# Kernel tuning notes

Hardware: AMD Instinct MI355X
Metric: run time of the kernel (lower is better)

Reference implementation:

```python
import jax, jax.numpy as jnp
import numpy as np

NEG_SLOPE = 0.2  # PyG GATConv leaky_relu slope
ENC_HEADS = 4


def _layernorm(x, g, b):
    mu = jnp.mean(x, axis=-1, keepdims=True)
    var = jnp.var(x, axis=-1, keepdims=True)
    return (x - mu) * jax.lax.rsqrt(var + 1e-5) * g + b


def _gat(x, src, dst, W, a_src, a_dst, bias, concat, num_nodes):
    """PyG-style GATConv: per-edge attention, scatter-softmax over dst, scatter-add."""
    heads, out = a_src.shape
    xl = (x @ W).reshape(-1, heads, out)              # (M, H, O)
    s = jnp.einsum('mho,ho->mh', xl, a_src)           # alpha_src per node
    d = jnp.einsum('mho,ho->mh', xl, a_dst)           # alpha_dst per node
    e = jax.nn.leaky_relu(s[src] + d[dst], NEG_SLOPE)  # (Etot, H)
    m = jax.lax.stop_gradient(jax.ops.segment_max(e, dst, num_segments=num_nodes))
    ee = jnp.exp(e - m[dst])
    denom = jax.ops.segment_sum(ee, dst, num_segments=num_nodes)
    alpha = ee / (denom[dst] + 1e-16)                 # scatter-softmax
    out_v = jax.ops.segment_sum(xl[src] * alpha[:, :, None], dst, num_segments=num_nodes)
    if concat:
        out_v = out_v.reshape(num_nodes, heads * out)
    else:
        out_v = out_v.mean(axis=1)
    return out_v + bias


def setup_inputs() -> dict:
    key = jax.random.key(0)
    ks = jax.random.split(key, 20)
    B, T, N, Ch, Cc = 4, 12, 10000, 8, 8
    H, GOUT, HOR, E = 128, 64, 24, 160000
    s = lambda k, shp: (jax.random.normal(k, shp, jnp.float32) * 0.05)
    return {
        'x_hist': jax.random.normal(ks[0], (B, T, N, Ch), jnp.float32),
        'x_cov': jax.random.normal(ks[1], (B, T, N, Cc), jnp.float32),
        'edge_index': jax.random.randint(ks[2], (2, E), 0, N, dtype=jnp.int32),
        'enc_in_W': s(ks[3], (Ch + Cc, H)), 'enc_in_b': jnp.zeros((H,), jnp.float32),
        'Wq': s(ks[4], (H, H)), 'Wk': s(ks[5], (H, H)), 'Wv': s(ks[6], (H, H)), 'Wo': s(ks[7], (H, H)),
        'ln1_g': jnp.ones((H,), jnp.float32), 'ln1_b': jnp.zeros((H,), jnp.float32),
        'ffn_W1': s(ks[8], (H, 2 * H)), 'ffn_b1': jnp.zeros((2 * H,), jnp.float32),
        'ffn_W2': s(ks[9], (2 * H, H)), 'ffn_b2': jnp.zeros((H,), jnp.float32),
        'ln2_g': jnp.ones((H,), jnp.float32), 'ln2_b': jnp.zeros((H,), jnp.float32),
        'gat1_W': s(ks[10], (H, H)), 'gat1_asrc': s(ks[11], (4, 32)), 'gat1_adst': s(ks[12], (4, 32)),
        'gat1_b': jnp.zeros((H,), jnp.float32),
        'gat2_W': s(ks[13], (H, GOUT)), 'gat2_asrc': s(ks[14], (1, GOUT)), 'gat2_adst': s(ks[15], (1, GOUT)),
        'gat2_b': jnp.zeros((GOUT,), jnp.float32),
        'out_W': s(ks[16], (GOUT, HOR)), 'out_b': jnp.zeros((HOR,), jnp.float32),
    }


def reference(x_hist, x_cov, edge_index, enc_in_W, enc_in_b, Wq, Wk, Wv, Wo,
              ln1_g, ln1_b, ffn_W1, ffn_b1, ffn_W2, ffn_b2, ln2_g, ln2_b,
              gat1_W, gat1_asrc, gat1_adst, gat1_b,
              gat2_W, gat2_asrc, gat2_adst, gat2_b, out_W, out_b):
    B, T, N, _ = x_hist.shape
    dh = Wq.shape[1] // ENC_HEADS
    # encoder: concat covariates, permute to (B, N, T, F)
    x = jnp.transpose(jnp.concatenate([x_hist, x_cov], axis=-1), (0, 2, 1, 3))
    h = x @ enc_in_W + enc_in_b                        # (B,N,T,H)
    q = (h @ Wq).reshape(B, N, T, ENC_HEADS, dh)
    k = (h @ Wk).reshape(B, N, T, ENC_HEADS, dh)
    v = (h @ Wv).reshape(B, N, T, ENC_HEADS, dh)
    logits = jnp.einsum('bnqhd,bnkhd->bnhqk', q, k) / jnp.sqrt(jnp.float32(dh))
    attn = jax.nn.softmax(logits, axis=-1)
    ao = jnp.einsum('bnhqk,bnkhd->bnqhd', attn, v).reshape(B, N, T, -1) @ Wo
    h = _layernorm(h + ao, ln1_g, ln1_b)
    f = jax.nn.relu(h @ ffn_W1 + ffn_b1) @ ffn_W2 + ffn_b2
    h = _layernorm(h + f, ln2_g, ln2_b)
    h = h[:, :, -1, :].reshape(B * N, -1)              # collapse time -> (B*N, H)
    # batched edge index (block-diagonal) + self loops (PyG default)
    M = B * N
    offs = jnp.arange(B, dtype=edge_index.dtype) * N
    src = (edge_index[0][None, :] + offs[:, None]).reshape(-1)
    dst = (edge_index[1][None, :] + offs[:, None]).reshape(-1)
    loops = jnp.arange(M, dtype=edge_index.dtype)
    src = jnp.concatenate([src, loops])
    dst = jnp.concatenate([dst, loops])
    g1 = jax.nn.elu(_gat(h, src, dst, gat1_W, gat1_asrc, gat1_adst, gat1_b, True, M))
    g2 = _gat(g1, src, dst, gat2_W, gat2_asrc, gat2_adst, gat2_b, False, M)
    y = g2.reshape(B, N, -1) @ out_W + out_b           # (B, N, horizon)
    return jnp.transpose(y, (0, 2, 1))                 # (B, horizon, N)
```

## Files before the change

### kernel.cpp

```cpp
#include <hip/hip_runtime.h>
#include <hip/hip_bf16.h>

#define DEV static __device__ __forceinline__

constexpr int BB = 4;
constexpr int TT = 12;
constexpr int NN = 10000;
constexpr int FD = 16;
constexpr int HD = 128;
constexpr int NH = 4;
constexpr int DH = 32;
constexpr int FF = 256;
constexpr int GO = 64;
constexpr int HR = 24;
constexpr int EE = 160000;
constexpr int MM = BB * NN;

typedef unsigned short bvec8 __attribute__((ext_vector_type(8)));
typedef unsigned short usvec4 __attribute__((ext_vector_type(4)));
typedef float fvec4 __attribute__((ext_vector_type(4)));
typedef short bs8 __attribute__((ext_vector_type(8)));

DEV float lrelu(float x) { return x >= 0.f ? x : 0.2f * x; }

DEV float b2f(unsigned short u) {
  union { unsigned int i; float f; } x; x.i = ((unsigned int)u) << 16; return x.f;
}
DEV unsigned short f2b(float f) {
  union { float f; unsigned int i; } x; x.f = f;
  unsigned int r = x.i + 0x7FFFu + ((x.i >> 16) & 1u);
  return (unsigned short)(r >> 16);
}
DEV void up2(unsigned int u, float& lo, float& hi) {
  union { unsigned int i; float f; } a, b;
  a.i = u << 16; b.i = u & 0xFFFF0000u;
  lo = a.f; hi = b.f;
}

DEV fvec4 mfma16(bs8 a, bs8 b, fvec4 c) {
  return __builtin_amdgcn_mfma_f32_16x16x32_bf16(a, b, c, 0, 0, 0);
}

__global__ __launch_bounds__(256) void k_prep(
    const float* __restrict__ Wq, const float* __restrict__ Wk,
    const float* __restrict__ Wv, const float* __restrict__ Wo,
    const float* __restrict__ encW, const float* __restrict__ encB,
    const float* __restrict__ W1, const float* __restrict__ fb1,
    const float* __restrict__ W2, const float* __restrict__ fb2,
    const float* __restrict__ l1g, const float* __restrict__ l1b,
    const float* __restrict__ l2g, const float* __restrict__ l2b,
    const float* __restrict__ gW1,
    unsigned short* __restrict__ Mu, unsigned short* __restrict__ Pw,
    unsigned short* __restrict__ W1F, unsigned short* __restrict__ W2F,
    unsigned short* __restrict__ encWF, unsigned short* __restrict__ gW1F,
    float* __restrict__ encBf, float* __restrict__ fb1f, float* __restrict__ fb2f,
    float* __restrict__ l1gf, float* __restrict__ l1bf,
    float* __restrict__ l2gf, float* __restrict__ l2bf)
{
  int idx = blockIdx.x * 256 + threadIdx.x;
  if (idx < 65536) {
    int e = idx & 7, lane = (idx >> 3) & 63, kk = (idx >> 9) & 3, nt = idx >> 11;
    int i = kk*32 + (lane >> 4)*8 + e;
    int q = nt*16 + (lane & 15);
    int h = q >> 7, c = q & 127;
    float a = 0.f;
    #pragma unroll 8
    for (int d = 0; d < DH; ++d)
      a += Wq[i*HD + h*DH + d] * Wk[c*HD + h*DH + d];
    Mu[idx] = f2b(a);
  } else if (idx < 131072) {
    int g2 = idx - 65536;
    int e = g2 & 7, lane = (g2 >> 3) & 63, kk = (g2 >> 9) & 15, nt = g2 >> 13;
    int q = kk*32 + (lane >> 4)*8 + e;
    int j = nt*16 + (lane & 15);
    int h = q >> 7, i = q & 127;
    float a = 0.f;
    #pragma unroll 8
    for (int d = 0; d < DH; ++d)
      a += Wv[i*HD + h*DH + d] * Wo[(h*DH + d)*HD + j];
    Pw[g2] = f2b(a);
  } else if (idx < 163840) {
    int g = idx - 131072;
    int e = g & 7, lane = (g >> 3) & 63, kk = (g >> 9) & 3, nt = g >> 11;
    int k = kk*32 + (lane >> 4)*8 + e;
    int n = nt*16 + (lane & 15);
    W1F[g] = f2b(W1[k*FF + n]);
  } else if (idx < 196608) {
    int g = idx - 163840;
    int e = g & 7, lane = (g >> 3) & 63, kk = (g >> 9) & 7, nt = g >> 12;
    int k = kk*32 + (lane >> 4)*8 + e;
    int n = nt*16 + (lane & 15);
    W2F[g] = f2b(W2[k*HD + n]);
  } else if (idx < 200704) {
    int g = idx - 196608;
    int e = g & 7, lane = (g >> 3) & 63, nt = g >> 9;
    int k = (lane >> 4)*8 + e;
    int n = nt*16 + (lane & 15);
    encWF[g] = (k < FD) ? f2b(encW[k*HD + n]) : (unsigned short)0;
  } else if (idx < 217088) {
    int g = idx - 200704;
    int e = g & 7, lane = (g >> 3) & 63, kk = (g >> 9) & 3, nt = g >> 11;
    int k = kk*32 + (lane >> 4)*8 + e;
    int n = nt*16 + (lane & 15);
    gW1F[g] = f2b(gW1[k*HD + n]);
  } else if (idx < 217216) { int t = idx - 217088; encBf[t] = encB[t]; }
  else if (idx < 217472)   { int t = idx - 217216; fb1f[t] = fb1[t]; }
  else if (idx < 217600)   { int t = idx - 217472; fb2f[t] = fb2[t]; }
  else if (idx < 217728)   { int t = idx - 217600; l1gf[t] = l1g[t]; }
  else if (idx < 217856)   { int t = idx - 217728; l1bf[t] = l1b[t]; }
  else if (idx < 217984)   { int t = idx - 217856; l2gf[t] = l2g[t]; }
  else                     { int t = idx - 217984; l2bf[t] = l2b[t]; }
}

__global__ __launch_bounds__(256) void k_xform(
    const float* __restrict__ xh, const float* __restrict__ xc,
    const unsigned short* __restrict__ MuF, const unsigned short* __restrict__ PwF,
    const unsigned short* __restrict__ W1F, const unsigned short* __restrict__ W2F,
    const unsigned short* __restrict__ encWF, const unsigned short* __restrict__ gW1F,
    const float* __restrict__ encBf,
    const float* __restrict__ fb1f, const float* __restrict__ fb2f,
    const float* __restrict__ l1gf, const float* __restrict__ l1bf,
    const float* __restrict__ l2gf, const float* __restrict__ l2bf,
    const float* __restrict__ asrc, const float* __restrict__ adrc,
    unsigned short* __restrict__ xl1B, float* __restrict__ s1, float* __restrict__ d1)
{
  __shared__ __align__(16) char big[26112];
  __shared__ unsigned short hlastB[8*136];
  __shared__ float lgaw[8][NH][TT];
  __shared__ __align__(16) char regB[8704];

  unsigned short* hsB = (unsigned short*)big;
  float* r1F = (float*)big;
  float* h1s = (float*)(big + 4224);
  unsigned short* h1B = (unsigned short*)(big + 8448);
  float* r2F = (float*)(big + 8448);
  unsigned short* f1B = (unsigned short*)(big + 12672);

  unsigned short* xB  = (unsigned short*)regB;
  unsigned short* usB = (unsigned short*)regB;
  unsigned short* wB  = (unsigned short*)regB;
  float* xlF = (float*)regB;

  const int tid  = threadIdx.x;
  const int w    = tid >> 6;
  const int lane = tid & 63;
  const int m0   = blockIdx.x * 8;
  const int arow = lane & 15, akg = lane >> 4;
  const int ar8  = arow & 7;

  #pragma unroll
  for (int k = 0; k < 6; ++k) {
    int idx = tid + k*256;
    int f = idx & 15, rest = idx >> 4;
    int nl = rest & 7, t = rest >> 3;
    int m = m0 + nl, b = m / NN, n = m - b*NN;
    float v = (f < 8) ? xh[(((size_t)b*TT + t)*NN + n)*8 + f]
                      : xc[(((size_t)b*TT + t)*NN + n)*8 + (f - 8)];
    xB[(t*8 + nl)*40 + f] = f2b(v);
  }
  #pragma unroll
  for (int k = 0; k < 6; ++k) {
    int idx = tid + k*256;
    xB[(idx >> 4)*40 + 16 + (idx & 15)] = 0;
  }
  __syncthreads();

  {
    const bs8* ef = (const bs8*)encWF;
    bs8 b0 = ef[(2*w + 0)*64 + lane];
    bs8 b1 = ef[(2*w + 1)*64 + lane];
    int drow = akg*4, dc = arow;
    int j0 = (2*w + 0)*16 + dc, j1 = (2*w + 1)*16 + dc;
    float eb0 = encBf[j0], eb1 = encBf[j1];
    fvec4 z4 = {0.f, 0.f, 0.f, 0.f};
    #pragma unroll
    for (int mt = 0; mt < 6; ++mt) {
      bs8 af = *(const bs8*)&xB[(mt*16 + arow)*40 + akg*8];
      fvec4 d0 = mfma16(af, b0, z4);
      fvec4 d1 = mfma16(af, b1, z4);
      #pragma unroll
      for (int reg = 0; reg < 4; ++reg) {
        int gr = mt*16 + drow + reg;
        int t = gr >> 3, nl = gr & 7;
        float v0 = d0[reg] + eb0, v1 = d1[reg] + eb1;
        unsigned short s0 = f2b(v0), s1v = f2b(v1);
        hsB[(nl*12 + t)*136 + j0] = s0;
        hsB[(nl*12 + t)*136 + j1] = s1v;
        if (t == TT-1) {
          hlastB[nl*136 + j0] = s0;
          hlastB[nl*136 + j1] = s1v;
        }
      }
    }
  }
  __syncthreads();

  {
    bs8 af[4];
    #pragma unroll
    for (int kk = 0; kk < 4; ++kk)
      af[kk] = *(const bs8*)&hlastB[ar8*136 + kk*32 + akg*8];
    const bs8* bp = (const bs8*)MuF;
    fvec4 acc[8];
    #pragma unroll
    for (int n8 = 0; n8 < 8; ++n8) {
      int nt = w*8 + n8;
      const bs8* bq = bp + nt*256 + lane;
      fvec4 a4 = {0.f, 0.f, 0.f, 0.f};
      #pragma unroll
      for (int kk = 0; kk < 4; ++kk)
        a4 = mfma16(af[kk], bq[kk*64], a4);
      acc[n8] = a4;
    }
    __syncthreads();
    if (lane < 32) {
      int drow = akg*4, dc = arow;
      #pragma unroll
      for (int n8 = 0; n8 < 8; ++n8) {
        int col = (w*8 + n8)*16 + dc, hd = col >> 7, c = col & 127;
        #pragma unroll
        for (int reg = 0; reg < 4; ++reg)
          usB[((drow + reg)*4 + hd)*136 + c] = f2b(acc[n8][reg]);
      }
    }
  }
  __syncthreads();

  #pragma unroll
  for (int pass = 0; pass < 2; ++pass) {
    int item = pass*256 + tid;
    if (item < 384) {
      int nl = item / 48, p = item - nl*48, hd = p / 12, t = p - hd*12;
      const unsigned short* up = &usB[(nl*4 + hd)*136];
      float a = 0.f;
      for (int i8 = 0; i8 < 16; ++i8) {
        bvec8 hb8 = *(const bvec8*)&hsB[(nl*12 + t)*136 + i8*8];
        bvec8 ub8 = *(const bvec8*)&up[i8*8];
        a += b2f(hb8[0])*b2f(ub8[0]) + b2f(hb8[1])*b2f(ub8[1])
           + b2f(hb8[2])*b2f(ub8[2]) + b2f(hb8[3])*b2f(ub8[3])
           + b2f(hb8[4])*b2f(ub8[4]) + b2f(hb8[5])*b2f(ub8[5])
           + b2f(hb8[6])*b2f(ub8[6]) + b2f(hb8[7])*b2f(ub8[7]);
      }
      lgaw[nl][hd][t] = a * 0.17677669529663687f;
    }
  }
  __syncthreads();

  if (tid < 32) {
    int nl = tid >> 2, hd = tid & 3;
    float mx = -1e30f;
    #pragma unroll
    for (int t = 0; t < TT; ++t) mx = fmaxf(mx, lgaw[nl][hd][t]);
    float ex[TT], sm = 0.f;
    #pragma unroll
    for (int t = 0; t < TT; ++t) { ex[t] = expf(lgaw[nl][hd][t] - mx); sm += ex[t]; }
    float inv = 1.f / sm;
    #pragma unroll
    for (int t = 0; t < TT; ++t) lgaw[nl][hd][t] = ex[t] * inv;
  }
  __syncthreads();

  {
    int g = tid >> 7, j = tid & 127;
    #pragma unroll
    for (int r = 0; r < 4; ++r) {
      int nl = g*4 + r;
      float wacc[NH] = {0.f, 0.f, 0.f, 0.f};
      #pragma unroll
      for (int t = 0; t < TT; ++t) {
        float hv = b2f(hsB[(nl*12 + t)*136 + j]);
        #pragma unroll
        for (int hd = 0; hd < NH; ++hd) wacc[hd] += lgaw[nl][hd][t] * hv;
      }
      #pragma unroll
      for (int hd = 0; hd < NH; ++hd) wB[nl*520 + hd*128 + j] = f2b(wacc[hd]);
    }
  }
  __syncthreads();

  {
    fvec4 pacc0 = {0.f,0.f,0.f,0.f}, pacc1 = {0.f,0.f,0.f,0.f};
    const bs8* bp = (const bs8*)PwF;
    const bs8* bq0 = bp + (w*2 + 0)*1024 + lane;
    const bs8* bq1 = bp + (w*2 + 1)*1024 + lane;
    #pragma unroll
    for (int kk = 0; kk < 16; ++kk) {
      bs8 af = *(const bs8*)&wB[ar8*520 + kk*32 + akg*8];
      pacc0 = mfma16(af, bq0[kk*64], pacc0);
      pacc1 = mfma16(af, bq1[kk*64], pacc1);
    }
    __syncthreads();
    if (lane < 32) {
      int drow = akg*4, dc = arow;
      #pragma unroll
      for (int reg = 0; reg < 4; ++reg) {
        int nd = drow + reg;
        int c0 = (w*2 + 0)*16 + dc;
        int c1 = (w*2 + 1)*16 + dc;
        r1F[nd*132 + c0] = b2f(hlastB[nd*136 + c0]) + pacc0[reg];
        r1F[nd*132 + c1] = b2f(hlastB[nd*136 + c1]) + pacc1[reg];
      }
    }
  }
  __syncthreads();

  {
    int nd = tid >> 5, l32 = tid & 31;
    float v[4], s = 0.f, q = 0.f;
    #pragma unroll
    for (int k = 0; k < 4; ++k) {
      v[k] = r1F[nd*132 + l32 + k*32];
      s += v[k]; q += v[k]*v[k];
    }
    #pragma unroll
    for (int off = 16; off > 0; off >>= 1) { s += __shfl_xor(s, off); q += __shfl_xor(q, off); }
    float mu = s*(1.f/128.f), var = q*(1.f/128.f) - mu*mu, rs = rsqrtf(var + 1e-5f);
    #pragma unroll
    for (int k = 0; k < 4; ++k) {
      int c = l32 + k*32;
      float hv = (v[k] - mu)*rs*l1gf[c] + l1bf[c];
      h1s[nd*132 + c] = hv;
      h1B[nd*136 + c] = f2b(hv);
    }
  }
  __syncthreads();

  {
    bs8 af[4];
    #pragma unroll
    for (int kk = 0; kk < 4; ++kk)
      af[kk] = *(const bs8*)&h1B[ar8*136 + kk*32 + akg*8];
    const bs8* bp = (const bs8*)W1F;
    #pragma unroll
    for (int n4 = 0; n4 < 4; ++n4) {
      int nt = w*4 + n4;
      const bs8* bq = bp + nt*256 + lane;
      fvec4 a4 = {0.f, 0.f, 0.f, 0.f};
      #pragma unroll
      for (int kk = 0; kk < 4; ++kk)
        a4 = mfma16(af[kk], bq[kk*64], a4);
      if (lane < 32) {
        int drow = akg*4, dc = arow;
        int n = nt*16 + dc;
        float bias = fb1f[n];
        #pragma unroll
        for (int reg = 0; reg < 4; ++reg)
          f1B[(drow + reg)*264 + n] = f2b(fmaxf(a4[reg] + bias, 0.f));
      }
    }
  }
  __syncthreads();

  {
    const bs8* bp = (const bs8*)W2F;
    #pragma unroll
    for (int n2 = 0; n2 < 2; ++n2) {
      int nt = w*2 + n2;
      const bs8* bq = bp + nt*512 + lane;
      fvec4 a4 = {0.f, 0.f, 0.f, 0.f};
      #pragma unroll
      for (int kk = 0; kk < 8; ++kk) {
        bs8 af = *(const bs8*)&f1B[ar8*264 + kk*32 + akg*8];
        a4 = mfma16(af, bq[kk*64], a4);
      }
      if (lane < 32) {
        int drow = akg*4, dc = arow;
        int c = nt*16 + dc;
        float fb2v = fb2f[c];
        #pragma unroll
        for (int reg = 0; reg < 4; ++reg) {
          int nd = drow + reg;
          r2F[nd*132 + c] = h1s[nd*132 + c] + fb2v + a4[reg];
        }
      }
    }
  }
  __syncthreads();

  {
    int nd = tid >> 5, l32 = tid & 31;
    float v[4], s = 0.f, q = 0.f;
    #pragma unroll
    for (int k = 0; k < 4; ++k) {
      v[k] = r2F[nd*132 + l32 + k*32];
      s += v[k]; q += v[k]*v[k];
    }
    #pragma unroll
    for (int off = 16; off > 0; off >>= 1) { s += __shfl_xor(s, off); q += __shfl_xor(q, off); }
    float mu = s*(1.f/128.f), var = q*(1.f/128.f) - mu*mu, rs = rsqrtf(var + 1e-5f);
    #pragma unroll
    for (int k = 0; k < 4; ++k) {
      int c = l32 + k*32;
      hlastB[nd*136 + c] = f2b((v[k] - mu)*rs*l2gf[c] + l2bf[c]);
    }
  }
  __syncthreads();

  {
    bs8 af[4];
    #pragma unroll
    for (int kk = 0; kk < 4; ++kk)
      af[kk] = *(const bs8*)&hlastB[ar8*136 + kk*32 + akg*8];
    const bs8* bp = (const bs8*)gW1F;
    #pragma unroll
    for (int n2 = 0; n2 < 2; ++n2) {
      int nt = w*2 + n2;
      const bs8* bq = bp + nt*256 + lane;
      fvec4 a4 = {0.f, 0.f, 0.f, 0.f};
      #pragma unroll
      for (int kk = 0; kk < 4; ++kk)
        a4 = mfma16(af[kk], bq[kk*64], a4);
      if (lane < 32) {
        int drow = akg*4, dc = arow;
        int c = nt*16 + dc;
        #pragma unroll
        for (int reg = 0; reg < 4; ++reg)
          xlF[(drow + reg)*128 + c] = a4[reg];
      }
    }
  }
  __syncthreads();
  {
    fvec4 vv = ((const fvec4*)xlF)[tid];
    usvec4 sv;
    #pragma unroll
    for (int k = 0; k < 4; ++k) sv[k] = f2b(vv[k]);
    *(usvec4*)&xl1B[(size_t)m0*HD + tid*4] = sv;
    int nd = tid >> 5, l32 = tid & 31;
    float pa[4], pb[4];
    #pragma unroll
    for (int k = 0; k < 4; ++k) {
      float xv = xlF[nd*128 + l32 + k*32];
      pa[k] = xv * asrc[l32 + k*32];
      pb[k] = xv * adrc[l32 + k*32];
    }
    #pragma unroll
    for (int off = 16; off > 0; off >>= 1) {
      #pragma unroll
      for (int k = 0; k < 4; ++k) {
        pa[k] += __shfl_xor(pa[k], off);
        pb[k] += __shfl_xor(pb[k], off);
      }
    }
    if (l32 == 0) {
      int m = m0 + nd;
      #pragma unroll
      for (int k = 0; k < 4; ++k) {
        s1[m*NH + k] = pa[k];
        d1[m*NH + k] = pb[k];
      }
    }
  }
}

__global__ __launch_bounds__(256) void k_zero(int* __restrict__ cnt)
{
  int i = blockIdx.x * 256 + threadIdx.x;
  if (i < NN) cnt[i] = 0;
}

__global__ __launch_bounds__(256) void k_hist(const int* __restrict__ e1,
                                              int* __restrict__ cnt)
{
  int i = blockIdx.x * 256 + threadIdx.x;
  if (i < EE) atomicAdd(&cnt[e1[i]], 1);
}

__global__ __launch_bounds__(1024) void k_scan(const int* __restrict__ cnt,
                                               int* __restrict__ row_ptr,
                                               int* __restrict__ cur)
{
  __shared__ int sm[1024];
  int tid = threadIdx.x;
  int base = tid * 10;
  int loc[10];
  int s = 0;
  #pragma unroll
  for (int k = 0; k < 10; ++k) {
    int idx = base + k;
    int v = (idx < NN) ? cnt[idx] : 0;
    loc[k] = s;
    s += v;
  }
  sm[tid] = s;
  __syncthreads();
  for (int off = 1; off < 1024; off <<= 1) {
    int t = (tid >= off) ? sm[tid - off] : 0;
    __syncthreads();
    sm[tid] += t;
    __syncthreads();
  }
  int segbase = sm[tid] - s;
  #pragma unroll
  for (int k = 0; k < 10; ++k) {
    int idx = base + k;
    if (idx < NN) { int o = segbase + loc[k]; row_ptr[idx] = o; cur[idx] = o; }
  }
  if (tid == 1023) row_ptr[NN] = sm[1023];
}

__global__ __launch_bounds__(256) void k_scatter(const int* __restrict__ e0,
                                                 const int* __restrict__ e1,
                                                 int* __restrict__ cur,
                                                 int* __restrict__ ssrc)
{
  int i = blockIdx.x * 256 + threadIdx.x;
  if (i >= EE) return;
  int pos = atomicAdd(&cur[e1[i]], 1);
  ssrc[pos] = e0[i];
}

__global__ __launch_bounds__(64) void k_g1(
    const int* __restrict__ row_ptr, const int* __restrict__ ssrc,
    const unsigned short* __restrict__ xlB,
    const float* __restrict__ s1, const float* __restrict__ d1,
    const float* __restrict__ gb1, const float* __restrict__ gW2,
    const float* __restrict__ asr2, const float* __restrict__ adr2,
    unsigned short* __restrict__ xl2B, float* __restrict__ s2, float* __restrict__ d2)
{
  __shared__ float g1s[HD];
  int j = threadIdx.x, m = blockIdx.x, h = j >> 4;
  int b = m / NN, n = m - b * NN, boff = b * NN;
  float dh = d1[m*NH + h];
  int r0 = row_ptr[n], r1 = row_ptr[n+1];
  float acc0 = 0.f, acc1 = 0.f, dsum = 0.f;
  for (int e = r0; e < r1; ++e) {
    int src = ssrc[e] + boff;
    float ev = expf(lrelu(s1[src*NH + h] + dh));
    unsigned int u = *(const unsigned int*)&xlB[(size_t)src*HD + 2*j];
    float lo, hi; up2(u, lo, hi);
    acc0 += ev * lo; acc1 += ev * hi;
    dsum += ev;
  }
  {
    float es = expf(lrelu(s1[m*NH + h] + dh));
    unsigned int u = *(const unsigned int*)&xlB[(size_t)m*HD + 2*j];
    float lo, hi; up2(u, lo, hi);
    acc0 += es * lo; acc1 += es * hi;
    dsum += es;
  }
  float inv = 1.f / (dsum + 1e-16f);
  float v0 = acc0 * inv + gb1[2*j];
  float v1 = acc1 * inv + gb1[2*j + 1];
  g1s[2*j]     = v0 > 0.f ? v0 : expm1f(v0);
  g1s[2*j + 1] = v1 > 0.f ? v1 : expm1f(v1);
  __syncthreads();
  float a = 0.f;
  for (int i = 0; i < HD; ++i) a += g1s[i] * gW2[i*GO + j];
  xl2B[(size_t)m*GO + j] = f2b(a);
  float pa = a * asr2[j], pb = a * adr2[j];
  #pragma unroll
  for (int off = 32; off > 0; off >>= 1) { pa += __shfl_xor(pa, off); pb += __shfl_xor(pb, off); }
  if (j == 0) { s2[m] = pa; d2[m] = pb; }
}

__global__ __launch_bounds__(64) void k_g2(
    const int* __restrict__ row_ptr, const int* __restrict__ ssrc,
    const unsigned short* __restrict__ xl2B,
    const float* __restrict__ s2, const float* __restrict__ d2,
    const float* __restrict__ gb2, const float* __restrict__ oW, const float* __restrict__ ob,
    float* __restrict__ y)
{
  __shared__ float g2s[GO];
  int j = threadIdx.x, m = blockIdx.x;
  int b = m / NN, n = m - b * NN, boff = b * NN;
  float d2m = d2[m];
  int r0 = row_ptr[n], r1 = row_ptr[n+1];
  float acc = 0.f, dsum = 0.f;
  for (int e = r0; e < r1; ++e) {
    int src = ssrc[e] + boff;
    float ev = expf(lrelu(s2[src] + d2m));
    acc  += ev * b2f(xl2B[(size_t)src*GO + j]);
    dsum += ev;
  }
  float es = expf(lrelu(s2[m] + d2m));
  acc  += es * b2f(xl2B[(size_t)m*GO + j]);
  dsum += es;
  g2s[j] = acc / (dsum + 1e-16f) + gb2[j];
  __syncthreads();
  if (j < HR) {
    float a = ob[j];
    #pragma unroll
    for (int o2 = 0; o2 < GO; ++o2) a += g2s[o2] * oW[o2*HR + j];
    y[((size_t)b*HR + j)*NN + n] = a;
  }
}

extern "C" void kernel_launch(void* const* d_in, const int* in_sizes, int n_in,
                              void* d_out, int out_size, void* d_ws, size_t ws_size,
                              hipStream_t stream)
{
  const int* ei = (const int*)d_in[2];
  const int* e0 = ei;
  const int* e1 = ei + EE;

  float* ws = (float*)d_ws;
  unsigned short* xl1B = (unsigned short*)ws;
  unsigned short* xl2B = (unsigned short*)(ws + 2560000);
  float* ovl = ws + 3840000;
  float* s1  = ws + 4200000;
  float* d1  = ws + 4360000;
  float* s2  = ws + 4520000;
  float* d2  = ws + 4560000;

  unsigned short* Mu    = (unsigned short*)ovl;
  unsigned short* Pw    = Mu + 65536;
  unsigned short* W1F   = Mu + 131072;
  unsigned short* W2F   = Mu + 163840;
  unsigned short* encWF = Mu + 196608;
  unsigned short* gW1F  = Mu + 200704;
  float* encBf = (float*)(Mu + 217088);
  float* fb1f  = encBf + 128;
  float* fb2f  = fb1f + 256;
  float* l1gf  = fb2f + 128;
  float* l1bf  = l1gf + 128;
  float* l2gf  = l1bf + 128;
  float* l2bf  = l2gf + 128;

  int* cnt     = (int*)ovl;
  int* row_ptr = cnt + 16384;
  int* cur     = cnt + 32768;
  int* ssrc    = cnt + 49152;

  k_prep<<<852, 256, 0, stream>>>(
      (const float*)d_in[5], (const float*)d_in[6], (const float*)d_in[7], (const float*)d_in[8],
      (const float*)d_in[3], (const float*)d_in[4], (const float*)d_in[11], (const float*)d_in[12],
      (const float*)d_in[13], (const float*)d_in[14], (const float*)d_in[9], (const float*)d_in[10],
      (const float*)d_in[15], (const float*)d_in[16], (const float*)d_in[17],
      Mu, Pw, W1F, W2F, encWF, gW1F,
      encBf, fb1f, fb2f, l1gf, l1bf, l2gf, l2bf);

  k_xform<<<MM/8, 256, 0, stream>>>(
      (const float*)d_in[0], (const float*)d_in[1],
      Mu, Pw, W1F, W2F, encWF, gW1F,
      encBf, fb1f, fb2f, l1gf, l1bf, l2gf, l2bf,
      (const float*)d_in[18], (const float*)d_in[19],
      xl1B, s1, d1);

  k_zero<<<(NN + 255)/256, 256, 0, stream>>>(cnt);
  k_hist<<<(EE + 255)/256, 256, 0, stream>>>(e1, cnt);
  k_scan<<<1, 1024, 0, stream>>>(cnt, row_ptr, cur);
  k_scatter<<<(EE + 255)/256, 256, 0, stream>>>(e0, e1, cur, ssrc);

  k_g1<<<MM, 64, 0, stream>>>(row_ptr, ssrc, xl1B, s1, d1,
      (const float*)d_in[20], (const float*)d_in[21],
      (const float*)d_in[22], (const float*)d_in[23],
      xl2B, s2, d2);

  k_g2<<<MM, 64, 0, stream>>>(row_ptr, ssrc, xl2B, s2, d2,
      (const float*)d_in[24], (const float*)d_in[25], (const float*)d_in[26],
      (float*)d_out);
}
```

Measured before the change: 280.7 us.

## Use MFMA for attention logits and pack two nodes per GAT block

The per-thread scalar bf16 dot products for temporal attention logits are replaced with 16x16 MFMA tiles per wave, discarding the unused rows and columns. The GAT aggregation kernels now process two nodes per 128-thread block to reduce block-launch overhead and raise occupancy. Their edge loops are unrolled by two so the gathers of two neighbours are in flight together. The MFMA path wastes most of each tile and relies on the lane mapping being correct.

Result: no change. 276.5 us (-1.5%).

```diff
diff --git a/kernel.cpp b/kernel.cpp
--- a/kernel.cpp
+++ b/kernel.cpp
@@ -226,22 +226,27 @@
   }
   __syncthreads();
 
-  #pragma unroll
-  for (int pass = 0; pass < 2; ++pass) {
-    int item = pass*256 + tid;
-    if (item < 384) {
-      int nl = item / 48, p = item - nl*48, hd = p / 12, t = p - hd*12;
-      const unsigned short* up = &usB[(nl*4 + hd)*136];
-      float a = 0.f;
-      for (int i8 = 0; i8 < 16; ++i8) {
-        bvec8 hb8 = *(const bvec8*)&hsB[(nl*12 + t)*136 + i8*8];
-        bvec8 ub8 = *(const bvec8*)&up[i8*8];
-        a += b2f(hb8[0])*b2f(ub8[0]) + b2f(hb8[1])*b2f(ub8[1])
-           + b2f(hb8[2])*b2f(ub8[2]) + b2f(hb8[3])*b2f(ub8[3])
-           + b2f(hb8[4])*b2f(ub8[4]) + b2f(hb8[5])*b2f(ub8[5])
-           + b2f(hb8[6])*b2f(ub8[6]) + b2f(hb8[7])*b2f(ub8[7]);
-      }
-      lgaw[nl][hd][t] = a * 0.17677669529663687f;
+  {
+    int ar12 = (arow < 12) ? arow : 0;
+    #pragma unroll
+    for (int r = 0; r < 2; ++r) {
+      int nl = w*2 + r;
+      const unsigned short* hb = &hsB[(nl*12 + ar12)*136 + akg*8];
+      const unsigned short* ub = &usB[(nl*4 + (arow & 3))*136 + akg*8];
+      fvec4 a4 = {0.f, 0.f, 0.f, 0.f};
+      #pragma unroll
+      for (int kk = 0; kk < 4; ++kk) {
+        bs8 af = *(const bs8*)&hb[kk*32];
+        bs8 bf = *(const bs8*)&ub[kk*32];
+        a4 = mfma16(af, bf, a4);
+      }
+      if (arow < 4) {
+        #pragma unroll
+        for (int reg = 0; reg < 4; ++reg) {
+          int t = akg*4 + reg;
+          if (t < TT) lgaw[nl][arow][t] = a4[reg] * 0.17677669529663687f;
+        }
+      }
     }
   }
   __syncthreads();
@@ -510,7 +515,7 @@
   ssrc[pos] = e0[i];
 }
 
-__global__ __launch_bounds__(64) void k_g1(
+__global__ __launch_bounds__(128) void k_g1(
     const int* __restrict__ row_ptr, const int* __restrict__ ssrc,
     const unsigned short* __restrict__ xlB,
     const float* __restrict__ s1, const float* __restrict__ d1,
@@ -518,16 +523,33 @@
     const float* __restrict__ asr2, const float* __restrict__ adr2,
     unsigned short* __restrict__ xl2B, float* __restrict__ s2, float* __restrict__ d2)
 {
-  __shared__ float g1s[HD];
-  int j = threadIdx.x, m = blockIdx.x, h = j >> 4;
+  __shared__ float g1s[2][HD];
+  int tid = threadIdx.x;
+  int half = tid >> 6;
+  int j = tid & 63;
+  int m = blockIdx.x * 2 + half;
+  int h = j >> 4;
   int b = m / NN, n = m - b * NN, boff = b * NN;
   float dh = d1[m*NH + h];
   int r0 = row_ptr[n], r1 = row_ptr[n+1];
   float acc0 = 0.f, acc1 = 0.f, dsum = 0.f;
-  for (int e = r0; e < r1; ++e) {
-    int src = ssrc[e] + boff;
-    float ev = expf(lrelu(s1[src*NH + h] + dh));
-    unsigned int u = *(const unsigned int*)&xlB[(size_t)src*HD + 2*j];
+  int e = r0;
+  for (; e + 2 <= r1; e += 2) {
+    int sa = ssrc[e] + boff, sb = ssrc[e+1] + boff;
+    float ka = s1[sa*NH + h], kb = s1[sb*NH + h];
+    unsigned int ua = *(const unsigned int*)&xlB[(size_t)sa*HD + 2*j];
+    unsigned int ub = *(const unsigned int*)&xlB[(size_t)sb*HD + 2*j];
+    float eva = expf(lrelu(ka + dh));
+    float evb = expf(lrelu(kb + dh));
+    float lo, hi;
+    up2(ua, lo, hi); acc0 += eva * lo; acc1 += eva * hi;
+    up2(ub, lo, hi); acc0 += evb * lo; acc1 += evb * hi;
+    dsum += eva + evb;
+  }
+  if (e < r1) {
+    int sa = ssrc[e] + boff;
+    float ev = expf(lrelu(s1[sa*NH + h] + dh));
+    unsigned int u = *(const unsigned int*)&xlB[(size_t)sa*HD + 2*j];
     float lo, hi; up2(u, lo, hi);
     acc0 += ev * lo; acc1 += ev * hi;
     dsum += ev;
@@ -542,11 +564,11 @@
   float inv = 1.f / (dsum + 1e-16f);
   float v0 = acc0 * inv + gb1[2*j];
   float v1 = acc1 * inv + gb1[2*j + 1];
-  g1s[2*j]     = v0 > 0.f ? v0 : expm1f(v0);
-  g1s[2*j + 1] = v1 > 0.f ? v1 : expm1f(v1);
+  g1s[half][2*j]     = v0 > 0.f ? v0 : expm1f(v0);
+  g1s[half][2*j + 1] = v1 > 0.f ? v1 : expm1f(v1);
   __syncthreads();
   float a = 0.f;
-  for (int i = 0; i < HD; ++i) a += g1s[i] * gW2[i*GO + j];
+  for (int i = 0; i < HD; ++i) a += g1s[half][i] * gW2[i*GO + j];
   xl2B[(size_t)m*GO + j] = f2b(a);
   float pa = a * asr2[j], pb = a * adr2[j];
   #pragma unroll
@@ -554,34 +576,48 @@
   if (j == 0) { s2[m] = pa; d2[m] = pb; }
 }
 
-__global__ __launch_bounds__(64) void k_g2(
+__global__ __launch_bounds__(128) void k_g2(
     const int* __restrict__ row_ptr, const int* __restrict__ ssrc,
     const unsigned short* __restrict__ xl2B,
     const float* __restrict__ s2, const float* __restrict__ d2,
     const float* __restrict__ gb2, const float* __restrict__ oW, const float* __restrict__ ob,
     float* __restrict__ y)
 {
-  __shared__ float g2s[GO];
-  int j = threadIdx.x, m = blockIdx.x;
+  __shared__ float g2s[2][GO];
+  int tid = threadIdx.x;
+  int half = tid >> 6;
+  int j = tid & 63;
+  int m = blockIdx.x * 2 + half;
   int b = m / NN, n = m - b * NN, boff = b * NN;
   float d2m = d2[m];
   int r0 = row_ptr[n], r1 = row_ptr[n+1];
   float acc = 0.f, dsum = 0.f;
-  for (int e = r0; e < r1; ++e) {
-    int src = ssrc[e] + boff;
-    float ev = expf(lrelu(s2[src] + d2m));
-    acc  += ev * b2f(xl2B[(size_t)src*GO + j]);
+  int e = r0;
+  for (; e + 2 <= r1; e += 2) {
+    int sa = ssrc[e] + boff, sb = ssrc[e+1] + boff;
+    float ka = s2[sa], kb = s2[sb];
+    unsigned short xa = xl2B[(size_t)sa*GO + j];
+    unsigned short xb = xl2B[(size_t)sb*GO + j];
+    float eva = expf(lrelu(ka + d2m));
+    float evb = expf(lrelu(kb + d2m));
+    acc  += eva * b2f(xa) + evb * b2f(xb);
+    dsum += eva + evb;
+  }
+  if (e < r1) {
+    int sa = ssrc[e] + boff;
+    float ev = expf(lrelu(s2[sa] + d2m));
+    acc  += ev * b2f(xl2B[(size_t)sa*GO + j]);
     dsum += ev;
   }
   float es = expf(lrelu(s2[m] + d2m));
   acc  += es * b2f(xl2B[(size_t)m*GO + j]);
   dsum += es;
-  g2s[j] = acc / (dsum + 1e-16f) + gb2[j];
+  g2s[half][j] = acc / (dsum + 1e-16f) + gb2[j];
   __syncthreads();
   if (j < HR) {
     float a = ob[j];
     #pragma unroll
-    for (int o2 = 0; o2 < GO; ++o2) a += g2s[o2] * oW[o2*HR + j];
+    for (int o2 = 0; o2 < GO; ++o2) a += g2s[half][o2] * oW[o2*HR + j];
     y[((size_t)b*HR + j)*NN + n] = a;
   }
 }
@@ -642,12 +678,12 @@
   k_scan<<<1, 1024, 0, stream>>>(cnt, row_ptr, cur);
   k_scatter<<<(EE + 255)/256, 256, 0, stream>>>(e0, e1, cur, ssrc);
 
-  k_g1<<<MM, 64, 0, stream>>>(row_ptr, ssrc, xl1B, s1, d1,
+  k_g1<<<MM/2, 128, 0, stream>>>(row_ptr, ssrc, xl1B, s1, d1,
       (const float*)d_in[20], (const float*)d_in[21],
       (const float*)d_in[22], (const float*)d_in[23],
       xl2B, s2, d2);
 
-  k_g2<<<MM, 64, 0, stream>>>(row_ptr, ssrc, xl2B, s2, d2,
+  k_g2<<<MM/2, 128, 0, stream>>>(row_ptr, ssrc, xl2B, s2, d2,
       (const float*)d_in[24], (const float*)d_in[25], (const float*)d_in[26],
       (float*)d_out);
 }
```
